# Optimization experiments

Measured on AMD Instinct MI355X. Metric: run time of the kernel, lower is better.

The kernel has to match this reference:

```python
import jax, jax.numpy as jnp
import numpy as np

B, S, DIM = 2, 1024, 2048
H, NOPE, ROPE_D, VD = 16, 128, 64, 128
QKD = NOPE + ROPE_D  # 192
BASE = 10000
NEG_INF = -1e9


def _rope_cos_sin(seq_len, start_pos=0):
    # theta: [ROPE_D//2]
    theta = 1.0 / (BASE ** (jnp.arange(0, ROPE_D, 2, dtype=jnp.float32) / ROPE_D))
    pos = jnp.arange(start_pos, start_pos + seq_len, dtype=jnp.float32)
    ang = pos[:, None] * theta[None, :]  # [s, ROPE_D//2]
    return jnp.cos(ang), jnp.sin(ang)


def _apply_rope(x, cos, sin):
    # x: [b, s, h, d]; cos/sin: [s, d//2]
    b, s, h, d = x.shape
    xs = x.astype(jnp.float32).reshape(b, s, h, d // 2, 2)
    c = cos[None, :, None, :]
    sn = sin[None, :, None, :]
    out = jnp.stack([xs[..., 0] * c - xs[..., 1] * sn,
                     xs[..., 1] * c + xs[..., 0] * sn], axis=-1)
    return out.reshape(b, s, h, d).astype(x.dtype)


def setup_inputs() -> dict:
    key = jax.random.key(0)
    ks = jax.random.split(key, 6)
    x = jax.random.normal(ks[0], (B, S, DIM), dtype=jnp.float32)
    sc = lambda fan_in: 1.0 / np.sqrt(fan_in)
    Wq = jax.random.normal(ks[1], (DIM, H * QKD), dtype=jnp.float32) * sc(DIM)
    Wk = jax.random.normal(ks[2], (DIM, H * QKD), dtype=jnp.float32) * sc(DIM)
    Wv = jax.random.normal(ks[3], (DIM, H * VD), dtype=jnp.float32) * sc(DIM)
    Wo = jax.random.normal(ks[4], (H * VD, DIM), dtype=jnp.float32) * sc(H * VD)
    bo = jnp.zeros((DIM,), dtype=jnp.float32)
    mask = jnp.where(jnp.tril(jnp.ones((S, S), dtype=bool)), 0.0, NEG_INF).astype(jnp.float32)
    return {"x": x, "Wq": Wq, "Wk": Wk, "Wv": Wv, "Wo": Wo, "bo": bo,
            "mask": mask, "start_pos": 0}


def reference(x, Wq, Wk, Wv, Wo, bo, mask, start_pos):
    b, s, _ = x.shape
    q = (x @ Wq).reshape(b, s, H, QKD)
    k = (x @ Wk).reshape(b, s, H, QKD)
    v = (x @ Wv).reshape(b, s, H, VD)
    q_nope, q_rope = q[..., :NOPE], q[..., NOPE:]
    k_nope, k_rope = k[..., :NOPE], k[..., NOPE:]
    cos, sin = _rope_cos_sin(s)  # input_pos=None -> positions 0..s-1
    q_rope = _apply_rope(q_rope, cos, sin)
    k_rope = _apply_rope(k_rope, cos, sin)
    q = jnp.concatenate([q_nope, q_rope], axis=-1)
    k = jnp.concatenate([k_nope, k_rope], axis=-1)
    # start_pos=0 prefill: cache[:end_pos] == k, v just written
    scale = QKD ** -0.5
    scores = jnp.einsum('bshd,bthd->bsht', q, k) * scale
    scores = scores + mask[:, None, :]  # mask.unsqueeze(1) on [b,s,h,t] broadcasting
    weights = jax.nn.softmax(scores.astype(jnp.float32), axis=-1).astype(x.dtype)
    c_v = jnp.einsum('bsht,bthd->bshd', weights, v)
    return c_v.reshape(b, s, H * VD) @ Wo + bo
```

## Files before the change

### kernel.cpp

```cpp
#include <hip/hip_runtime.h>


typedef __bf16 bf16;
typedef __bf16 bf16x8 __attribute__((ext_vector_type(8)));
typedef __bf16 bf16x4 __attribute__((ext_vector_type(4)));
typedef float  f32x4  __attribute__((ext_vector_type(4)));

#define DEVI __device__ __forceinline__

static constexpr int Bc = 2, Sc = 1024, DIMc = 2048, Hc = 16;
static constexpr int NOPEc = 128, QKDc = 192, VDc = 128;
static constexpr int NQ    = Hc * QKDc;
static constexpr int NCAT  = NQ + NQ + Hc*VDc;

__global__ __launch_bounds__(256) void k_prep(const float* __restrict__ x,
                                              const float* __restrict__ Wq, const float* __restrict__ Wk,
                                              const float* __restrict__ Wv, const float* __restrict__ Wo,
                                              bf16* __restrict__ xb, bf16* __restrict__ wcat,
                                              bf16* __restrict__ woT,
                                              float* __restrict__ cosT, float* __restrict__ sinT) {
    __shared__ float tile[64][68];
    const int yt = blockIdx.y, xt = blockIdx.x, tid = threadIdx.x;
    if (yt < 160) {
        const float* src; bf16* dst; int N, n0;
        if (yt < 48)       { src = Wq; N = 3072; n0 = yt * 64;         dst = wcat; }
        else if (yt < 96)  { src = Wk; N = 3072; n0 = (yt - 48) * 64;  dst = wcat + (size_t)3072 * 2048; }
        else if (yt < 128) { src = Wv; N = 2048; n0 = (yt - 96) * 64;  dst = wcat + (size_t)6144 * 2048; }
        else               { src = Wo; N = 2048; n0 = (yt - 128) * 64; dst = woT; }
        int k0 = xt * 64;
        int tr = tid >> 4, tc = (tid & 15) * 4;
#pragma unroll
        for (int i = 0; i < 4; i++) {
            int r = tr + i * 16;
            float4 v = *(const float4*)(src + (size_t)(k0 + r) * N + n0 + tc);
            tile[r][tc+0] = v.x; tile[r][tc+1] = v.y; tile[r][tc+2] = v.z; tile[r][tc+3] = v.w;
        }
        __syncthreads();
#pragma unroll
        for (int i = 0; i < 4; i++) {
            int n = tr + i * 16;
            bf16x4 o;
#pragma unroll
            for (int j = 0; j < 4; j++) o[j] = (bf16)tile[tc + j][n];
            *(bf16x4*)(dst + (size_t)(n0 + n) * 2048 + k0 + tc) = o;
        }
    } else if (yt < 224) {
        int i = (((yt - 160) * 32 + xt) * 256 + tid) * 8;
        float4 a = *(const float4*)(x + i);
        float4 b = *(const float4*)(x + i + 4);
        bf16x8 o;
        o[0]=(bf16)a.x; o[1]=(bf16)a.y; o[2]=(bf16)a.z; o[3]=(bf16)a.w;
        o[4]=(bf16)b.x; o[5]=(bf16)b.y; o[6]=(bf16)b.z; o[7]=(bf16)b.w;
        *(bf16x8*)(xb + i) = o;
    } else {
#pragma unroll
        for (int p = 0; p < 4; p++) {
            int idx = p * 8192 + xt * 256 + tid;
            int pos = idx >> 5, i = idx & 31;
            float theta = expf(-(float)i * (9.210340371976184f / 32.0f));
            float ang = (float)pos * theta;
            cosT[idx] = cosf(ang);
            sinT[idx] = sinf(ang);
        }
    }
}

__global__ __launch_bounds__(256) void k_rope2(bf16* __restrict__ qkv, const float* __restrict__ cosT,
                                               const float* __restrict__ sinT) {
    int bidx = blockIdx.x;
    int secbase = (bidx >= 1024) ? NQ : 0;
    int idx = (bidx & 1023) * 256 + threadIdx.x;
    int g = idx & 7, h = (idx >> 3) & 15, row = idx >> 7;
    int s = row & (Sc - 1);
    bf16* p = qkv + (size_t)row * NCAT + secbase + h * QKDc + NOPEc + g * 8;
    bf16x8 v = *(bf16x8*)p;
    const float* cp = cosT + s * 32 + g * 4;
    const float* sp = sinT + s * 32 + g * 4;
#pragma unroll
    for (int q = 0; q < 4; q++) {
        float x0 = (float)v[2*q], x1 = (float)v[2*q+1];
        float c = cp[q], sn = sp[q];
        v[2*q]   = (bf16)(x0 * c - x1 * sn);
        v[2*q+1] = (bf16)(x1 * c + x0 * sn);
    }
    *(bf16x8*)p = v;
}

__global__ __launch_bounds__(256) void k_vt(const bf16* __restrict__ qkv, bf16* __restrict__ vT) {
    int st = blockIdx.x, dt = blockIdx.y, bh = blockIdx.z;
    int b = bh >> 4, h = bh & 15;
    __shared__ bf16 tile[64][72];
    int r = threadIdx.x >> 3, c8 = (threadIdx.x & 7) * 8;
    const bf16* src = qkv + (size_t)(b * Sc + st * 64) * NCAT + 2 * NQ + h * VDc + dt * 64;
#pragma unroll
    for (int i = 0; i < 2; i++) {
        int rr = r + i * 32;
        *(bf16x8*)&tile[rr][c8] = *(const bf16x8*)(src + (size_t)rr * NCAT + c8);
    }
    __syncthreads();
    bf16* dst = vT + ((size_t)bh * 128 + dt * 64) * Sc + st * 64;
#pragma unroll
    for (int i = 0; i < 2; i++) {
        int rr = r + i * 32;
        bf16x8 o;
#pragma unroll
        for (int j = 0; j < 8; j++) o[j] = tile[c8 + j][rr];
        *(bf16x8*)(dst + (size_t)rr * Sc + c8) = o;
    }
}

DEVI void gload16(const bf16* g, bf16* l) {
    __builtin_amdgcn_global_load_lds((const __attribute__((address_space(1))) void*)g,
                                     (__attribute__((address_space(3))) void*)l, 16, 0, 0);
}

__global__ __launch_bounds__(512, 2) void k_gemm8(const bf16* __restrict__ A, const bf16* __restrict__ Bt,
                                                  bf16* __restrict__ C, int N, int K, int NCT) {
    __shared__ __align__(16) bf16 lds[2][2][2][256 * 32];
    const int tid = threadIdx.x;
    const int l = tid & 63, wid = tid >> 6;
    const int lg = l >> 4, lc = l & 15;
    const int wm = wid >> 2, wn = wid & 3;
    const int bid = blockIdx.x;
    const int xcd = bid & 7, g = bid >> 3;
    const int per = NCT >> 3;
    const int rt = g & 7, ct = xcd * per + (g >> 3);
    const int row0 = rt * 256, col0 = ct * 256;
    const int NT = K >> 6;

    const bf16* Abase = A  + (size_t)row0 * K;
    const bf16* Bbase = Bt + (size_t)col0 * K;

    size_t srcoff0, srcoff1;
    int ldsoff0, ldsoff1;
    {
        int li0 = tid,        r0 = li0 >> 2, u0 = li0 & 3;
        int li1 = 512 + tid,  r1 = li1 >> 2, u1 = li1 & 3;
        srcoff0 = (size_t)r0 * K + ((u0 ^ ((r0 >> 1) & 3)) << 3);  ldsoff0 = li0 * 8;
        srcoff1 = (size_t)r1 * K + ((u1 ^ ((r1 >> 1) & 3)) << 3);  ldsoff1 = li1 * 8;
    }

#define STAGE8(ab, ks, ktile, buf) { \
    const bf16* gb_ = ((ab) ? Bbase : Abase) + (ktile) * 64 + (ks) * 32; \
    bf16* lb_ = &lds[buf][ab][ks][0]; \
    gload16(gb_ + srcoff0, lb_ + ldsoff0); \
    gload16(gb_ + srcoff1, lb_ + ldsoff1); }

#define RD_A8(dst, P) { _Pragma("unroll") \
    for (int i_ = 0; i_ < 8; i_++) { \
        int row_ = wm * 128 + i_ * 16 + lc; \
        dst[i_] = *(const bf16x8*)((P) + row_ * 32 + ((lg ^ ((row_ >> 1) & 3)) << 3)); } }
#define RD_B4(dst, P) { _Pragma("unroll") \
    for (int fc_ = 0; fc_ < 4; fc_++) { \
        int row_ = wn * 64 + fc_ * 16 + lc; \
        dst[fc_] = *(const bf16x8*)((P) + row_ * 32 + ((lg ^ ((row_ >> 1) & 3)) << 3)); } }
#define MM32(Av, Bv) { _Pragma("unroll") \
    for (int i_ = 0; i_ < 8; i_++) _Pragma("unroll") \
        for (int fc_ = 0; fc_ < 4; fc_++) \
            acc[i_][fc_] = __builtin_amdgcn_mfma_f32_16x16x32_bf16(Av[i_], Bv[fc_], acc[i_][fc_], 0, 0, 0); }
#define BAR() { __builtin_amdgcn_s_barrier(); asm volatile("" ::: "memory"); }

    f32x4 acc[8][4] = {};
    bf16x8 aX[8], bX[4], aY[8], bY[4];

    STAGE8(0, 0, 0, 0); STAGE8(1, 0, 0, 0); STAGE8(0, 1, 0, 0); STAGE8(1, 1, 0, 0);
    asm volatile("s_waitcnt vmcnt(0)" ::: "memory");
    BAR();
    RD_A8(aX, &lds[0][0][0][0]);
    RD_B4(bX, &lds[0][1][0][0]);

    for (int kt = 0; kt < NT; ++kt) {
        const int cur = kt & 1, nxt = cur ^ 1;
        const bool notlast = (kt + 1 < NT);
        if (notlast) {
            STAGE8(0, 0, kt + 1, nxt); STAGE8(1, 0, kt + 1, nxt);
            STAGE8(0, 1, kt + 1, nxt); STAGE8(1, 1, kt + 1, nxt);
        }
        RD_A8(aY, &lds[cur][0][1][0]);
        RD_B4(bY, &lds[cur][1][1][0]);
        __builtin_amdgcn_s_setprio(1);
        MM32(aX, bX);
        __builtin_amdgcn_s_setprio(0);
        if (notlast) {
            asm volatile("s_waitcnt lgkmcnt(0)" ::: "memory");
            asm volatile("s_waitcnt vmcnt(0)" ::: "memory");
            BAR();
            RD_A8(aX, &lds[nxt][0][0][0]);
            RD_B4(bX, &lds[nxt][1][0][0]);
        } else {
            asm volatile("s_waitcnt lgkmcnt(0)" ::: "memory");
        }
        __builtin_amdgcn_s_setprio(1);
        MM32(aY, bY);
        __builtin_amdgcn_s_setprio(0);
    }
#undef STAGE8
#undef RD_A8
#undef RD_B4
#undef MM32
#undef BAR
#pragma unroll
    for (int m = 0; m < 8; m++)
#pragma unroll
        for (int fc = 0; fc < 4; fc++)
#pragma unroll
            for (int j = 0; j < 4; j++) {
                int r = row0 + wm * 128 + m * 16 + lg * 4 + j;
                int c = col0 + wn * 64 + fc * 16 + lc;
                C[(size_t)r * N + c] = (bf16)acc[m][fc][j];
            }
}

__global__ __launch_bounds__(512, 2) void k_gemmO(const bf16* __restrict__ A, const bf16* __restrict__ Bt,
                                                  float* __restrict__ C, const float* __restrict__ bias,
                                                  int N, int K) {
    __shared__ __align__(16) bf16 lds[2][2][2][128 * 32];
    const int tid = threadIdx.x;
    const int l = tid & 63, wid = tid >> 6;
    const int lg = l >> 4, lc = l & 15;
    const int wm = wid >> 2, wn = wid & 3;
    const int bid = blockIdx.x;
    const int xcd = bid & 7, g = bid >> 3;
    const int rt = g & 15, ct = xcd * 2 + (g >> 4);
    const int row0 = rt * 128, col0 = ct * 128;
    const int NT = K >> 6;

    const bf16* Abase = A  + (size_t)row0 * K;
    const bf16* Bbase = Bt + (size_t)col0 * K;

    size_t srcoff; int ldsoff;
    {
        int r0 = tid >> 2, u0 = tid & 3;
        srcoff = (size_t)r0 * K + ((u0 ^ ((r0 >> 1) & 3)) << 3);
        ldsoff = tid * 8;
    }

#define STAGEO(ab, ks, ktile, buf) { \
    const bf16* gb_ = ((ab) ? Bbase : Abase) + (ktile) * 64 + (ks) * 32; \
    gload16(gb_ + srcoff, &lds[buf][ab][ks][0] + ldsoff); }

    f32x4 acc[4][2] = {};

    STAGEO(0, 0, 0, 0); STAGEO(1, 0, 0, 0); STAGEO(0, 1, 0, 0); STAGEO(1, 1, 0, 0);
    asm volatile("s_waitcnt vmcnt(2)" ::: "memory");
    __builtin_amdgcn_s_barrier();
    asm volatile("" ::: "memory");

    for (int kt = 0; kt < NT; ++kt) {
        const int cur = kt & 1, nxt = cur ^ 1;
        const bool notlast = (kt + 1 < NT);
#pragma unroll
        for (int ph = 0; ph < 2; ph++) {
            const bf16* As_ = &lds[cur][0][ph][0];
            const bf16* Bs_ = &lds[cur][1][ph][0];
            bf16x8 aF[4], bB[2];
#pragma unroll
            for (int n = 0; n < 2; n++) {
                int row = wn * 32 + n * 16 + lc;
                bB[n] = *(const bf16x8*)(Bs_ + row * 32 + ((lg ^ ((row >> 1) & 3)) << 3));
            }
#pragma unroll
            for (int m = 0; m < 4; m++) {
                int row = wm * 64 + m * 16 + lc;
                aF[m] = *(const bf16x8*)(As_ + row * 32 + ((lg ^ ((row >> 1) & 3)) << 3));
            }
            if (notlast) {
                if (ph == 0) { STAGEO(0, 0, kt + 1, nxt); STAGEO(1, 0, kt + 1, nxt); }
                else         { STAGEO(0, 1, kt + 1, nxt); STAGEO(1, 1, kt + 1, nxt); }
            }
            __builtin_amdgcn_s_barrier();
            asm volatile("" ::: "memory");
            __builtin_amdgcn_s_setprio(1);
#pragma unroll
            for (int m = 0; m < 4; m++)
#pragma unroll
                for (int n = 0; n < 2; n++)
                    acc[m][n] = __builtin_amdgcn_mfma_f32_16x16x32_bf16(aF[m], bB[n], acc[m][n], 0, 0, 0);
            __builtin_amdgcn_s_setprio(0);
            if (notlast)          asm volatile("s_waitcnt vmcnt(2)" ::: "memory");
            else if (ph == 0)     asm volatile("s_waitcnt vmcnt(0)" ::: "memory");
            __builtin_amdgcn_s_barrier();
            asm volatile("" ::: "memory");
        }
    }
#undef STAGEO
#pragma unroll
    for (int m = 0; m < 4; m++)
#pragma unroll
        for (int n = 0; n < 2; n++)
#pragma unroll
            for (int j = 0; j < 4; j++) {
                int r = row0 + wm * 64 + m * 16 + lg * 4 + j;
                int c = col0 + wn * 32 + n * 16 + lc;
                C[(size_t)r * N + c] = acc[m][n][j] + bias[c];
            }
}

__global__ __launch_bounds__(256, 3) void k_attn(const bf16* __restrict__ qkv, const bf16* __restrict__ vT,
                                                 bf16* __restrict__ cv) {
    const int bid = blockIdx.x;
    const int xcd = bid & 7, g = bid >> 3;
    const int qt = (g & 32) ? (g & 15) : (15 - (g & 15));
    const int bh = xcd + 8 * (g >> 4);
    const int b = bh >> 4, h = bh & 15;
    const int tid = threadIdx.x, l = tid & 63, w = tid >> 6;
    const int lg = l >> 4, lc = l & 15;
    __shared__ __align__(16) bf16 Ks[64 * 192];
    __shared__ __align__(16) bf16 Vs[128 * 64];
    __shared__ __align__(16) bf16 Pl[4][16][72];
    const bf16* Qb = qkv + (size_t)b * Sc * NCAT + h * QKDc;
    const bf16* Kb = Qb + NQ;
    const bf16* Vt = vT + (size_t)bh * 128 * Sc;

    int sK[6];
#pragma unroll
    for (int r = 0; r < 6; r++) {
        int li = r * 256 + tid;
        int row = li / 24, c16 = li - row * 24;
        sK[r] = row * NCAT + ((c16 ^ (row & 7)) * 8);
    }
    int sV[4];
#pragma unroll
    for (int r = 0; r < 4; r++) {
        int li = r * 256 + tid;
        int row = li >> 3, c16 = li & 7;
        sV[r] = row * Sc + ((c16 ^ (row & 7)) * 8);
    }
    const int swz = lc & 7;

    bf16x8 qF[6];
    const int qrow = qt * 64 + w * 16 + lc;
#pragma unroll
    for (int kc = 0; kc < 6; kc++) qF[kc] = *(const bf16x8*)(Qb + (size_t)qrow * NCAT + kc * 32 + lg * 8);

    f32x4 acc[8] = {};
    float mrow[4] = {-1e30f, -1e30f, -1e30f, -1e30f};
    float lsum[4] = {0.f, 0.f, 0.f, 0.f};
    const float scale = 0.07216878364870323f;

#pragma unroll
    for (int r = 0; r < 6; r++) gload16(Kb + sK[r], Ks + (r * 256 + tid) * 8);

    for (int c = 0; c <= qt; ++c) {
        const int t0 = c * 64;
        __syncthreads();
#pragma unroll
        for (int r = 0; r < 4; r++) gload16(Vt + t0 + sV[r], Vs + (r * 256 + tid) * 8);
        f32x4 sc[4] = {};
#pragma unroll
        for (int nt = 0; nt < 4; nt++)
#pragma unroll
            for (int kc = 0; kc < 6; kc++) {
                bf16x8 kf = *(const bf16x8*)(Ks + (nt * 16 + lc) * 192 + (((kc * 4 + lg) ^ swz) * 8));
                sc[nt] = __builtin_amdgcn_mfma_f32_16x16x32_bf16(qF[kc], kf, sc[nt], 0, 0, 0);
            }
        __syncthreads();
        if (c < qt) {
#pragma unroll
            for (int r = 0; r < 6; r++) gload16(Kb + (size_t)(t0 + 64) * NCAT + sK[r], Ks + (r * 256 + tid) * 8);
        }
        float p[4][4];
        float cmax[4] = {-1e30f, -1e30f, -1e30f, -1e30f};
        const bool diag = (c == qt);
#pragma unroll
        for (int nt = 0; nt < 4; nt++)
#pragma unroll
            for (int j = 0; j < 4; j++) {
                float v = sc[nt][j] * scale;
                if (diag) {
                    int tg = t0 + nt * 16 + lc;
                    int rg = qt * 64 + w * 16 + lg * 4 + j;
                    if (tg > rg) v = -1e9f;
                }
                p[nt][j] = v;
                cmax[j] = fmaxf(cmax[j], v);
            }
#pragma unroll
        for (int j = 0; j < 4; j++)
#pragma unroll
            for (int d = 1; d < 16; d <<= 1) cmax[j] = fmaxf(cmax[j], __shfl_xor(cmax[j], d));
        float f[4];
#pragma unroll
        for (int j = 0; j < 4; j++) {
            float nm = fmaxf(mrow[j], cmax[j]);
            f[j] = __expf(mrow[j] - nm);
            mrow[j] = nm;
        }
        float psum[4] = {0.f, 0.f, 0.f, 0.f};
#pragma unroll
        for (int nt = 0; nt < 4; nt++)
#pragma unroll
            for (int j = 0; j < 4; j++) {
                p[nt][j] = __expf(p[nt][j] - mrow[j]);
                psum[j] += p[nt][j];
            }
#pragma unroll
        for (int j = 0; j < 4; j++) {
#pragma unroll
            for (int d = 1; d < 16; d <<= 1) psum[j] += __shfl_xor(psum[j], d);
            lsum[j] = lsum[j] * f[j] + psum[j];
        }
#pragma unroll
        for (int n = 0; n < 8; n++)
#pragma unroll
            for (int j = 0; j < 4; j++) acc[n][j] *= f[j];
#pragma unroll
        for (int nt = 0; nt < 4; nt++)
#pragma unroll
            for (int j = 0; j < 4; j++)
                Pl[w][lg * 4 + j][nt * 16 + lc] = (bf16)p[nt][j];
#pragma unroll
        for (int ks = 0; ks < 2; ks++) {
            bf16x8 aP = *(const bf16x8*)(&Pl[w][lc][ks * 32 + lg * 8]);
#pragma unroll
            for (int n = 0; n < 8; n++) {
                bf16x8 bV = *(const bf16x8*)(Vs + (n * 16 + lc) * 64 + (((ks * 4 + lg) ^ swz) * 8));
                acc[n] = __builtin_amdgcn_mfma_f32_16x16x32_bf16(aP, bV, acc[n], 0, 0, 0);
            }
        }
    }
#pragma unroll
    for (int j = 0; j < 4; j++) {
        float inv = 1.0f / lsum[j];
        int r = qt * 64 + w * 16 + lg * 4 + j;
#pragma unroll
        for (int n = 0; n < 8; n++) {
            float v = acc[n][j] * inv;
            cv[((size_t)(b * Sc + r) * Hc + h) * VDc + n * 16 + lc] = (bf16)v;
        }
    }
}

extern "C" void kernel_launch(void* const* d_in, const int* in_sizes, int n_in,
                              void* d_out, int out_size, void* d_ws, size_t ws_size,
                              hipStream_t stream) {
    const float* x  = (const float*)d_in[0];
    const float* Wq = (const float*)d_in[1];
    const float* Wk = (const float*)d_in[2];
    const float* Wv = (const float*)d_in[3];
    const float* Wo = (const float*)d_in[4];
    const float* bo = (const float*)d_in[5];
    float* out = (float*)d_out;
    char* ws = (char*)d_ws;

    bf16*  wcat = (bf16*)(ws + 0);
    bf16*  woT  = (bf16*)(ws + 33554432);
    bf16*  xb   = (bf16*)(ws + 41943040);
    bf16*  qkvb = (bf16*)(ws + 50331648);
    bf16*  cvb  = (bf16*)(ws + 83886080);
    bf16*  vTb  = (bf16*)(ws + 92274688);
    float* cosT = (float*)(ws + 100663296);
    float* sinT = (float*)(ws + 100794368);

    k_prep<<<dim3(32, 225), 256, 0, stream>>>(x, Wq, Wk, Wv, Wo, xb, wcat, woT, cosT, sinT);
    k_gemm8<<<256, 512, 0, stream>>>(xb, wcat, qkvb, NCAT, DIMc, NCAT / 256);
    k_rope2<<<2048, 256, 0, stream>>>(qkvb, cosT, sinT);
    k_vt<<<dim3(16, 2, 32), 256, 0, stream>>>(qkvb, vTb);
    k_attn<<<512, 256, 0, stream>>>(qkvb, vTb, cvb);
    k_gemmO<<<256, 512, 0, stream>>>(cvb, woT, out, bo, DIMc, DIMc);
}
```

Measured before the change: 159.0 us.

## Load GEMM B operand directly to registers and merge rope/V-transpose kernels

The QKV GEMM now stages only the A tile through LDS, while each wave loads its B fragments straight from global memory into registers one k-step ahead. This halves LDS usage and LDS traffic for B, and relaxes the vmcnt wait so the B loads can stay in flight. The cost is that B is reloaded by each of the two wm waves instead of being shared through LDS. Separately, the rope and V-transpose kernels are fused into one launch to save a kernel launch.

```diff
diff --git a/kernel.cpp b/kernel.cpp
--- a/kernel.cpp
+++ b/kernel.cpp
@@ -65,47 +65,48 @@
     }
 }
 
-__global__ __launch_bounds__(256) void k_rope2(bf16* __restrict__ qkv, const float* __restrict__ cosT,
-                                               const float* __restrict__ sinT) {
-    int bidx = blockIdx.x;
-    int secbase = (bidx >= 1024) ? NQ : 0;
-    int idx = (bidx & 1023) * 256 + threadIdx.x;
-    int g = idx & 7, h = (idx >> 3) & 15, row = idx >> 7;
-    int s = row & (Sc - 1);
-    bf16* p = qkv + (size_t)row * NCAT + secbase + h * QKDc + NOPEc + g * 8;
-    bf16x8 v = *(bf16x8*)p;
-    const float* cp = cosT + s * 32 + g * 4;
-    const float* sp = sinT + s * 32 + g * 4;
-#pragma unroll
-    for (int q = 0; q < 4; q++) {
-        float x0 = (float)v[2*q], x1 = (float)v[2*q+1];
-        float c = cp[q], sn = sp[q];
-        v[2*q]   = (bf16)(x0 * c - x1 * sn);
-        v[2*q+1] = (bf16)(x1 * c + x0 * sn);
-    }
-    *(bf16x8*)p = v;
-}
-
-__global__ __launch_bounds__(256) void k_vt(const bf16* __restrict__ qkv, bf16* __restrict__ vT) {
-    int st = blockIdx.x, dt = blockIdx.y, bh = blockIdx.z;
-    int b = bh >> 4, h = bh & 15;
-    __shared__ bf16 tile[64][72];
-    int r = threadIdx.x >> 3, c8 = (threadIdx.x & 7) * 8;
-    const bf16* src = qkv + (size_t)(b * Sc + st * 64) * NCAT + 2 * NQ + h * VDc + dt * 64;
-#pragma unroll
-    for (int i = 0; i < 2; i++) {
-        int rr = r + i * 32;
-        *(bf16x8*)&tile[rr][c8] = *(const bf16x8*)(src + (size_t)rr * NCAT + c8);
-    }
-    __syncthreads();
-    bf16* dst = vT + ((size_t)bh * 128 + dt * 64) * Sc + st * 64;
-#pragma unroll
-    for (int i = 0; i < 2; i++) {
-        int rr = r + i * 32;
-        bf16x8 o;
-#pragma unroll
-        for (int j = 0; j < 8; j++) o[j] = tile[c8 + j][rr];
-        *(bf16x8*)(dst + (size_t)rr * Sc + c8) = o;
+__global__ __launch_bounds__(256) void k_ropevt(bf16* __restrict__ qkv, const float* __restrict__ cosT,
+                                                const float* __restrict__ sinT, bf16* __restrict__ vT) {
+    const int bidx = blockIdx.x, tid = threadIdx.x;
+    if (bidx < 2048) {
+        int secbase = (bidx >= 1024) ? NQ : 0;
+        int idx = (bidx & 1023) * 256 + tid;
+        int g = idx & 7, h = (idx >> 3) & 15, row = idx >> 7;
+        int s = row & (Sc - 1);
+        bf16* p = qkv + (size_t)row * NCAT + secbase + h * QKDc + NOPEc + g * 8;
+        bf16x8 v = *(bf16x8*)p;
+        const float* cp = cosT + s * 32 + g * 4;
+        const float* sp = sinT + s * 32 + g * 4;
+#pragma unroll
+        for (int q = 0; q < 4; q++) {
+            float x0 = (float)v[2*q], x1 = (float)v[2*q+1];
+            float c = cp[q], sn = sp[q];
+            v[2*q]   = (bf16)(x0 * c - x1 * sn);
+            v[2*q+1] = (bf16)(x1 * c + x0 * sn);
+        }
+        *(bf16x8*)p = v;
+    } else {
+        __shared__ bf16 tile[64][72];
+        const int vb = bidx - 2048;
+        const int st = vb & 15, dt = (vb >> 4) & 1, bh = vb >> 5;
+        const int b = bh >> 4, h = bh & 15;
+        int r = tid >> 3, c8 = (tid & 7) * 8;
+        const bf16* src = qkv + (size_t)(b * Sc + st * 64) * NCAT + 2 * NQ + h * VDc + dt * 64;
+#pragma unroll
+        for (int i = 0; i < 2; i++) {
+            int rr = r + i * 32;
+            *(bf16x8*)&tile[rr][c8] = *(const bf16x8*)(src + (size_t)rr * NCAT + c8);
+        }
+        __syncthreads();
+        bf16* dst = vT + ((size_t)bh * 128 + dt * 64) * Sc + st * 64;
+#pragma unroll
+        for (int i = 0; i < 2; i++) {
+            int rr = r + i * 32;
+            bf16x8 o;
+#pragma unroll
+            for (int j = 0; j < 8; j++) o[j] = tile[c8 + j][rr];
+            *(bf16x8*)(dst + (size_t)rr * Sc + c8) = o;
+        }
     }
 }
 
@@ -116,7 +117,7 @@
 
 __global__ __launch_bounds__(512, 2) void k_gemm8(const bf16* __restrict__ A, const bf16* __restrict__ Bt,
                                                   bf16* __restrict__ C, int N, int K, int NCT) {
-    __shared__ __align__(16) bf16 lds[2][2][2][256 * 32];
+    __shared__ __align__(16) bf16 lds[2][2][256 * 32];
     const int tid = threadIdx.x;
     const int l = tid & 63, wid = tid >> 6;
     const int lg = l >> 4, lc = l & 15;
@@ -129,7 +130,7 @@
     const int NT = K >> 6;
 
     const bf16* Abase = A  + (size_t)row0 * K;
-    const bf16* Bbase = Bt + (size_t)col0 * K;
+    const bf16* Bl = Bt + (size_t)(col0 + wn * 64 + lc) * K + lg * 8;
 
     size_t srcoff0, srcoff1;
     int ldsoff0, ldsoff1;
@@ -140,20 +141,19 @@
         srcoff1 = (size_t)r1 * K + ((u1 ^ ((r1 >> 1) & 3)) << 3);  ldsoff1 = li1 * 8;
     }
 
-#define STAGE8(ab, ks, ktile, buf) { \
-    const bf16* gb_ = ((ab) ? Bbase : Abase) + (ktile) * 64 + (ks) * 32; \
-    bf16* lb_ = &lds[buf][ab][ks][0]; \
-    gload16(gb_ + srcoff0, lb_ + ldsoff0); \
-    gload16(gb_ + srcoff1, lb_ + ldsoff1); }
+#define STAGEA(ks, ktile, buf) { \
+    const bf16* ga_ = Abase + (ktile) * 64 + (ks) * 32; \
+    gload16(ga_ + srcoff0, &lds[buf][ks][0] + ldsoff0); \
+    gload16(ga_ + srcoff1, &lds[buf][ks][0] + ldsoff1); }
+
+#define LOADB(dst, ks, ktile) { _Pragma("unroll") \
+    for (int fc_ = 0; fc_ < 4; fc_++) \
+        dst[fc_] = *(const bf16x8*)(Bl + (size_t)(fc_ * 16) * K + (ktile) * 64 + (ks) * 32); }
 
 #define RD_A8(dst, P) { _Pragma("unroll") \
     for (int i_ = 0; i_ < 8; i_++) { \
         int row_ = wm * 128 + i_ * 16 + lc; \
         dst[i_] = *(const bf16x8*)((P) + row_ * 32 + ((lg ^ ((row_ >> 1) & 3)) << 3)); } }
-#define RD_B4(dst, P) { _Pragma("unroll") \
-    for (int fc_ = 0; fc_ < 4; fc_++) { \
-        int row_ = wn * 64 + fc_ * 16 + lc; \
-        dst[fc_] = *(const bf16x8*)((P) + row_ * 32 + ((lg ^ ((row_ >> 1) & 3)) << 3)); } }
 #define MM32(Av, Bv) { _Pragma("unroll") \
     for (int i_ = 0; i_ < 8; i_++) _Pragma("unroll") \
         for (int fc_ = 0; fc_ < 4; fc_++) \
@@ -161,42 +161,39 @@
 #define BAR() { __builtin_amdgcn_s_barrier(); asm volatile("" ::: "memory"); }
 
     f32x4 acc[8][4] = {};
-    bf16x8 aX[8], bX[4], aY[8], bY[4];
-
-    STAGE8(0, 0, 0, 0); STAGE8(1, 0, 0, 0); STAGE8(0, 1, 0, 0); STAGE8(1, 1, 0, 0);
+    bf16x8 aX[8], aY[8], bX[4], bY[4];
+
+    STAGEA(0, 0, 0); STAGEA(1, 0, 0);
+    LOADB(bX, 0, 0); LOADB(bY, 1, 0);
     asm volatile("s_waitcnt vmcnt(0)" ::: "memory");
     BAR();
-    RD_A8(aX, &lds[0][0][0][0]);
-    RD_B4(bX, &lds[0][1][0][0]);
+    RD_A8(aX, &lds[0][0][0]);
 
     for (int kt = 0; kt < NT; ++kt) {
         const int cur = kt & 1, nxt = cur ^ 1;
         const bool notlast = (kt + 1 < NT);
-        if (notlast) {
-            STAGE8(0, 0, kt + 1, nxt); STAGE8(1, 0, kt + 1, nxt);
-            STAGE8(0, 1, kt + 1, nxt); STAGE8(1, 1, kt + 1, nxt);
-        }
-        RD_A8(aY, &lds[cur][0][1][0]);
-        RD_B4(bY, &lds[cur][1][1][0]);
+        if (notlast) { STAGEA(0, kt + 1, nxt); STAGEA(1, kt + 1, nxt); }
+        RD_A8(aY, &lds[cur][1][0]);
         __builtin_amdgcn_s_setprio(1);
         MM32(aX, bX);
         __builtin_amdgcn_s_setprio(0);
+        if (notlast) LOADB(bX, 0, kt + 1);
         if (notlast) {
             asm volatile("s_waitcnt lgkmcnt(0)" ::: "memory");
-            asm volatile("s_waitcnt vmcnt(0)" ::: "memory");
+            asm volatile("s_waitcnt vmcnt(4)" ::: "memory");
             BAR();
-            RD_A8(aX, &lds[nxt][0][0][0]);
-            RD_B4(bX, &lds[nxt][1][0][0]);
+            RD_A8(aX, &lds[nxt][0][0]);
         } else {
             asm volatile("s_waitcnt lgkmcnt(0)" ::: "memory");
         }
         __builtin_amdgcn_s_setprio(1);
         MM32(aY, bY);
         __builtin_amdgcn_s_setprio(0);
-    }
-#undef STAGE8
+        if (notlast) LOADB(bY, 1, kt + 1);
+    }
+#undef STAGEA
+#undef LOADB
 #undef RD_A8
-#undef RD_B4
 #undef MM32
 #undef BAR
 #pragma unroll
@@ -454,8 +451,7 @@
 
     k_prep<<<dim3(32, 225), 256, 0, stream>>>(x, Wq, Wk, Wv, Wo, xb, wcat, woT, cosT, sinT);
     k_gemm8<<<256, 512, 0, stream>>>(xb, wcat, qkvb, NCAT, DIMc, NCAT / 256);
-    k_rope2<<<2048, 256, 0, stream>>>(qkvb, cosT, sinT);
-    k_vt<<<dim3(16, 2, 32), 256, 0, stream>>>(qkvb, vTb);
+    k_ropevt<<<3072, 256, 0, stream>>>(qkvb, cosT, sinT, vTb);
     k_attn<<<512, 256, 0, stream>>>(qkvb, vTb, cvb);
     k_gemmO<<<256, 512, 0, stream>>>(cvb, woT, out, bo, DIMc, DIMc);
 }
```

Result: slower. 174.3 us (+9.6%).
